# Optimization experiments

Measured on AMD Instinct MI355X. Metric: run time of the kernel, lower is better.

The kernel has to match this reference:

```python
import jax, jax.numpy as jnp
import numpy as np

EPS = 1e-5
NUM_GROUPS = 32
NUM_HEADS = 8

def group_norm(x, w, b):
    # x: (B, C, H, W), 32 groups, affine per-channel
    B, C, H, W = x.shape
    xg = x.reshape(B, NUM_GROUPS, C // NUM_GROUPS, H, W)
    mu = xg.mean(axis=(2, 3, 4), keepdims=True)
    var = xg.var(axis=(2, 3, 4), keepdims=True)
    xn = ((xg - mu) * jax.lax.rsqrt(var + EPS)).reshape(B, C, H, W)
    return xn * w[None, :, None, None] + b[None, :, None, None]

def conv1x1(x, w, b):
    # 1x1 conv == per-pixel linear; w: (out, in), x: (B, C, H, W)
    return jnp.einsum('oc,bchw->bohw', w, x) + b[None, :, None, None]

def setup_inputs() -> dict:
    key = jax.random.key(0)
    ks = jax.random.split(key, 4)
    B, C, H, W = 2, 512, 64, 64
    s = 1.0 / np.sqrt(C)
    return {
        'x': jax.random.normal(ks[0], (B, C, H, W), jnp.float32),
        'gn_w': jnp.ones((C,), jnp.float32),
        'gn_b': jnp.zeros((C,), jnp.float32),
        'wq': jax.random.normal(ks[1], (C, C), jnp.float32) * s,
        'bq': jnp.zeros((C,), jnp.float32),
        'wkv': jax.random.normal(ks[2], (2 * C, C), jnp.float32) * s,
        'bkv': jnp.zeros((2 * C,), jnp.float32),
        'wo': jax.random.normal(ks[3], (C, C), jnp.float32) * s,
        'bo': jnp.zeros((C,), jnp.float32),
    }

def reference(x, gn_w, gn_b, wq, bq, wkv, bkv, wo, bo):
    B, C, H, W = x.shape
    hd = C // NUM_HEADS  # head_dim
    residual = x
    x_norm = group_norm(x, gn_w, gn_b)
    q = conv1x1(x_norm, wq, bq).reshape(B, NUM_HEADS, hd, H * W)
    kv = conv1x1(x_norm, wkv, bkv)
    k, v = jnp.split(kv, 2, axis=1)
    k = k.reshape(B, NUM_HEADS, hd, H * W)
    v = v.reshape(B, NUM_HEADS, hd, H * W)
    scale = hd ** (-0.5)
    attn = jnp.einsum('bhdi,bhdj->bhij', q, k) * scale
    attn = jax.nn.softmax(attn, axis=-1)
    out = jnp.einsum('bhij,bhdj->bhdi', attn, v).reshape(B, C, H, W)
    out = conv1x1(out, wo, bo)
    return out + residual
```

## Files before the change

### kernel.cpp

```cpp
#include <hip/hip_runtime.h>
#include <cmath>

typedef __bf16 bf16x8 __attribute__((ext_vector_type(8)));
typedef __bf16 bf16x4 __attribute__((ext_vector_type(4)));
typedef float  f32x4  __attribute__((ext_vector_type(4)));
typedef unsigned uint2_ev __attribute__((ext_vector_type(2)));

static __device__ __forceinline__ f32x4 mfma16(bf16x8 a, bf16x8 b, f32x4 c) {
    return __builtin_amdgcn_mfma_f32_16x16x32_bf16(a, b, c, 0, 0, 0);
}

static __device__ __forceinline__ float fast_exp2(float x) {
#if __has_builtin(__builtin_amdgcn_exp2f)
    return __builtin_amdgcn_exp2f(x);
#else
    return exp2f(x);
#endif
}

static __device__ __forceinline__ void quad_swap(unsigned &a, unsigned &b) {
#if __has_builtin(__builtin_amdgcn_permlane32_swap) && __has_builtin(__builtin_amdgcn_permlane16_swap)
    uint2_ev r32 = __builtin_amdgcn_permlane32_swap(a, b, false, false);
    uint2_ev r16 = __builtin_amdgcn_permlane16_swap(r32[0], r32[1], false, false);
    a = r16[0]; b = r16[1];
#else
    asm volatile("v_permlane32_swap_b32 %0, %1\n\t"
                 "v_permlane16_swap_b32 %0, %1"
                 : "+v"(a), "+v"(b));
#endif
}

static __device__ __forceinline__ void gload_lds16(const void* g, void* l) {
    __builtin_amdgcn_global_load_lds((const __attribute__((address_space(1))) void*)g,
                                     (__attribute__((address_space(3))) void*)l, 16, 0, 0);
}

#define OFF_STATS 0
#define OFF_BEFF  1024
#define OFF_W     16384
#define OFF_XNT   (4u*1024*1024)
#define OFF_QKT   (OFF_XNT + 8u*1024*1024)
#define OFF_V     (OFF_QKT + 16u*1024*1024)
#define OFF_OP    (OFF_V + 8u*1024*1024)
#define CHUNK_O   4194304u
#define CHUNK_L   65536u

__global__ __launch_bounds__(256) void gn_fuse(const float* __restrict__ x,
                                               float* __restrict__ stats,
                                               __bf16* __restrict__ xT) {
    int p0 = blockIdx.x * 64, c0 = blockIdx.y * 64, b = blockIdx.z;
    int tid = threadIdx.x, lane = tid & 63, wave = tid >> 6;
    __shared__ float t[64][68];
    __shared__ float red[4][8];
    float acc_s[4] = {0.f,0.f,0.f,0.f}, acc_ss[4] = {0.f,0.f,0.f,0.f};
    const int rr = tid >> 4;
    const int p4 = (tid & 15) * 4;
    #pragma unroll
    for (int i = 0; i < 4; ++i) {
        int cc = rr + 16*i;
        float4 v = *(const float4*)&x[((size_t)(b*512 + c0 + cc) << 12) + p0 + p4];
        *(float4*)&t[cc][p4] = v;
        acc_s[i]  += v.x + v.y + v.z + v.w;
        acc_ss[i] += v.x*v.x + v.y*v.y + v.z*v.z + v.w*v.w;
    }
    #pragma unroll
    for (int g = 0; g < 4; ++g) {
        #pragma unroll
        for (int off = 1; off < 64; off <<= 1) {
            acc_s[g]  += __shfl_xor(acc_s[g],  off);
            acc_ss[g] += __shfl_xor(acc_ss[g], off);
        }
    }
    if (lane == 0) {
        #pragma unroll
        for (int g = 0; g < 4; ++g) { red[wave][g*2] = acc_s[g]; red[wave][g*2+1] = acc_ss[g]; }
    }
    __syncthreads();
    if (tid < 8) {
        float v0 = red[0][tid] + red[1][tid] + red[2][tid] + red[3][tid];
        int g = (b << 5) + (c0 >> 4) + (tid >> 1);
        atomicAdd(&stats[g*2 + (tid & 1)], v0);
    }
    const int ch = tid & 7;
    #pragma unroll
    for (int w = 0; w < 2; ++w) {
        int pp = (tid >> 3) + 32*w;
        __bf16 ob[8];
        #pragma unroll
        for (int e = 0; e < 8; ++e) ob[e] = (__bf16)t[ch*8 + e][pp];
        *(bf16x8*)&xT[((size_t)(b*4096 + p0 + pp) << 9) + c0 + ch*8] = *(bf16x8*)ob;
    }
}

__global__ __launch_bounds__(256) void prep_w(const float* __restrict__ wq,
                                              const float* __restrict__ wkv,
                                              const float* __restrict__ wo,
                                              const float* __restrict__ bq,
                                              const float* __restrict__ bkv,
                                              const float* __restrict__ stats,
                                              const float* __restrict__ gw,
                                              const float* __restrict__ gb,
                                              __bf16* __restrict__ wS,
                                              __bf16* __restrict__ wo_bf,
                                              float* __restrict__ beff) {
    const int b = blockIdx.y, bx = blockIdx.x;
    const int tid = threadIdx.x, lane = tid & 63, wave = tid >> 6;
    if (bx >= 48) {
        if (b) return;
        int r0 = (bx - 48) * 32;
        #pragma unroll
        for (int ps = 0; ps < 8; ++ps) {
            int row = r0 + ps*4 + wave;
            __bf16 obuf[8];
            #pragma unroll
            for (int e = 0; e < 8; ++e) obuf[e] = (__bf16)wo[(size_t)row*512 + lane*8 + e];
            *(bf16x8*)&wo_bf[(size_t)row*512 + lane*8] = *(bf16x8*)obuf;
        }
        return;
    }
    __shared__ float sS[512], sT[512];
    for (int c = tid; c < 512; c += 256) {
        int g = (b << 5) + (c >> 4);
        float mu   = stats[g*2] * (1.f/65536.f);
        float var  = stats[g*2+1] * (1.f/65536.f) - mu*mu;
        float rstd = rsqrtf(var + 1e-5f);
        float s = rstd * gw[c];
        sS[c] = s;
        sT[c] = gb[c] - mu * s;
    }
    __syncthreads();
    int r0 = bx * 32;
    #pragma unroll
    for (int ps = 0; ps < 8; ++ps) {
        int row = r0 + ps*4 + wave;
        const float* Wrow = (row < 512) ? (wq + (size_t)row*512) : (wkv + (size_t)(row-512)*512);
        float bias0 = (row < 512) ? bq[row] : bkv[row - 512];
        float bp = 0.f;
        __bf16 obuf[8];
        #pragma unroll
        for (int e = 0; e < 8; ++e) {
            int c = lane*8 + e;
            float wv_ = Wrow[c];
            obuf[e] = (__bf16)(wv_ * sS[c]);
            bp += wv_ * sT[c];
        }
        *(bf16x8*)&wS[((size_t)b*1536 + row)*512 + lane*8] = *(bf16x8*)obuf;
        #pragma unroll
        for (int off = 1; off < 64; off <<= 1) bp += __shfl_xor(bp, off);
        if (lane == 0) beff[b*1536 + row] = bias0 + bp;
    }
}

__global__ __launch_bounds__(256) void gemm128_kernel(
    const __bf16* __restrict__ A, const __bf16* __restrict__ B,
    const float* __restrict__ bias, int nsplit,
    float scale0, void* __restrict__ out, void* __restrict__ outV,
    int N, int K, long long strideA, long long strideB, long long strideO,
    long long strideV, int biasStride) {
    const int bz = blockIdx.z;
    A += strideA * bz;
    B += strideB * bz;
    const float* bb = bias + (size_t)bz * biasStride;
    const int m0 = blockIdx.x * 128, n0 = blockIdx.y * 128;
    const int tid = threadIdx.x, lane = tid & 63, wave = tid >> 6;
    const int quad = lane >> 4, l16 = lane & 15;
    const int wm = (wave >> 1) * 64, wn = (wave & 1) * 64;

    __shared__ __attribute__((aligned(16))) __bf16 lds_a[2][128][64];
    __shared__ __attribute__((aligned(16))) __bf16 lds_b[2][128][64];

    f32x4 acc[4][4];
    #pragma unroll
    for (int mt = 0; mt < 4; ++mt)
        #pragma unroll
        for (int nt = 0; nt < 4; ++nt)
            #pragma unroll
            for (int r = 0; r < 4; ++r) acc[mt][nt][r] = 0.f;

    const int myrow = (wave << 3) + (lane >> 3);
    const int mych  = ((lane & 7) ^ (myrow & 7)) << 3;
    const __bf16* Ab = A + (size_t)(m0 + myrow) * K + mych;
    const __bf16* Bb = B + (size_t)(n0 + myrow) * K + mych;

    auto stage = [&](int buf, int kt) {
        char* la = (char*)(&lds_a[buf][0][0]) + (wave << 10);
        char* lb = (char*)(&lds_b[buf][0][0]) + (wave << 10);
        #pragma unroll
        for (int i = 0; i < 4; ++i) {
            gload_lds16(Ab + kt + (size_t)(32*i) * K, la + i*4096);
            gload_lds16(Bb + kt + (size_t)(32*i) * K, lb + i*4096);
        }
    };

    stage(0, 0);
    const int NK = K >> 6;
    for (int k8 = 0; k8 < NK; ++k8) {
        __syncthreads();
        const int cur = k8 & 1;
        if (k8 + 1 < NK) stage(cur ^ 1, (k8 + 1) << 6);
        #pragma unroll
        for (int kh = 0; kh < 2; ++kh) {
            bf16x8 af[4], bfr[4];
            #pragma unroll
            for (int mt = 0; mt < 4; ++mt)
                af[mt] = *(const bf16x8*)&lds_a[cur][wm + mt*16 + l16][(((kh<<2)|quad) ^ (l16 & 7)) * 8];
            #pragma unroll
            for (int nt = 0; nt < 4; ++nt)
                bfr[nt] = *(const bf16x8*)&lds_b[cur][wn + nt*16 + l16][(((kh<<2)|quad) ^ (l16 & 7)) * 8];
            #pragma unroll
            for (int mt = 0; mt < 4; ++mt)
                #pragma unroll
                for (int nt = 0; nt < 4; ++nt)
                    acc[mt][nt] = mfma16(af[mt], bfr[nt], acc[mt][nt]);
        }
    }

    if (n0 < 1024) {
        #pragma unroll
        for (int mt = 0; mt < 4; ++mt) {
            const int mrow = m0 + wm + mt*16 + quad*4;
            #pragma unroll
            for (int nt = 0; nt < 4; ++nt) {
                const int ncol = n0 + wn + nt*16 + l16;
                #pragma unroll
                for (int r = 0; r < 4; ++r) {
                    const int m = mrow + r;
                    float val = acc[mt][nt][r] + bb[ncol];
                    if (ncol < nsplit) val *= scale0;
                    ((__bf16*)out)[(size_t)strideO * bz + (size_t)m * N + ncol] = (__bf16)val;
                }
            }
        }
    } else {
        __syncthreads();
        __bf16* T = (__bf16*)lds_a;
        #pragma unroll
        for (int mt = 0; mt < 4; ++mt) {
            const int pl  = wm + mt*16 + quad*4;
            const int pc  = pl >> 3;
            const int hlf = (pl >> 2) & 1;
            #pragma unroll
            for (int nt = 0; nt < 4; ++nt) {
                const int cl = wn + nt*16 + l16;
                const int ncol = n0 + cl;
                __bf16 ob[4];
                #pragma unroll
                for (int r = 0; r < 4; ++r)
                    ob[r] = (__bf16)(acc[mt][nt][r] + bb[ncol]);
                *(bf16x4*)&T[cl*128 + ((pc ^ (cl & 15)) << 3) + hlf*4] = *(bf16x4*)ob;
            }
        }
        __syncthreads();
        const int pch = tid & 15;
        __bf16* vvb = (__bf16*)outV + (size_t)strideV * bz;
        #pragma unroll
        for (int pass = 0; pass < 8; ++pass) {
            const int cl = pass*16 + (tid >> 4);
            bf16x8 vv8 = *(const bf16x8*)&T[cl*128 + ((pch ^ (cl & 15)) << 3)];
            *(bf16x8*)&vvb[(size_t)(n0 - 1024 + cl) * 4096 + m0 + pch*8] = vv8;
        }
    }
}

template<int OUT_F32, int HAS_RES>
__global__ __launch_bounds__(256) void gemm64_kernel(
    const __bf16* __restrict__ A, const __bf16* __restrict__ B,
    const float* __restrict__ bias, const float* __restrict__ res,
    void* __restrict__ out,
    int N, int K, long long strideA, long long strideB, long long strideO, int biasStride) {
    const int bz = blockIdx.z;
    A += strideA * bz;
    B += strideB * bz;
    const float* bb = bias + (size_t)bz * biasStride;
    const int m0 = blockIdx.x * 64, n0 = blockIdx.y * 128;
    const int tid = threadIdx.x, lane = tid & 63, wave = tid >> 6;
    const int quad = lane >> 4, l16 = lane & 15;
    const int wn = wave * 32;

    __shared__ __attribute__((aligned(16))) __bf16 lds_a[2][64][64];
    __shared__ __attribute__((aligned(16))) __bf16 lds_b[2][128][64];

    f32x4 acc[4][2];
    #pragma unroll
    for (int mt = 0; mt < 4; ++mt)
        #pragma unroll
        for (int nt = 0; nt < 2; ++nt)
            #pragma unroll
            for (int r = 0; r < 4; ++r) acc[mt][nt][r] = 0.f;

    const int myrow = (wave << 3) + (lane >> 3);
    const int mych  = ((lane & 7) ^ (myrow & 7)) << 3;
    const __bf16* Ab = A + (size_t)(m0 + myrow) * K + mych;
    const __bf16* Bb = B + (size_t)(n0 + myrow) * K + mych;

    auto stage = [&](int buf, int kt) {
        char* la = (char*)(&lds_a[buf][0][0]) + (wave << 10);
        char* lb = (char*)(&lds_b[buf][0][0]) + (wave << 10);
        #pragma unroll
        for (int i = 0; i < 2; ++i)
            gload_lds16(Ab + kt + (size_t)(32*i) * K, la + i*4096);
        #pragma unroll
        for (int i = 0; i < 4; ++i)
            gload_lds16(Bb + kt + (size_t)(32*i) * K, lb + i*4096);
    };

    stage(0, 0);
    const int NK = K >> 6;
    for (int k8 = 0; k8 < NK; ++k8) {
        __syncthreads();
        const int cur = k8 & 1;
        if (k8 + 1 < NK) stage(cur ^ 1, (k8 + 1) << 6);
        #pragma unroll
        for (int kh = 0; kh < 2; ++kh) {
            bf16x8 af[4], bfr[2];
            #pragma unroll
            for (int mt = 0; mt < 4; ++mt)
                af[mt] = *(const bf16x8*)&lds_a[cur][mt*16 + l16][(((kh<<2)|quad) ^ (l16 & 7)) * 8];
            #pragma unroll
            for (int nt = 0; nt < 2; ++nt)
                bfr[nt] = *(const bf16x8*)&lds_b[cur][wn + nt*16 + l16][(((kh<<2)|quad) ^ (l16 & 7)) * 8];
            #pragma unroll
            for (int mt = 0; mt < 4; ++mt)
                #pragma unroll
                for (int nt = 0; nt < 2; ++nt)
                    acc[mt][nt] = mfma16(af[mt], bfr[nt], acc[mt][nt]);
        }
    }

    #pragma unroll
    for (int mt = 0; mt < 4; ++mt) {
        const int mrow = m0 + mt*16 + quad*4;
        #pragma unroll
        for (int nt = 0; nt < 2; ++nt) {
            const int ncol = n0 + wn + nt*16 + l16;
            #pragma unroll
            for (int r = 0; r < 4; ++r) {
                const int m = mrow + r;
                float val = acc[mt][nt][r] + bb[m];
                const size_t idx = (size_t)strideO * bz + (size_t)m * N + ncol;
                if constexpr (HAS_RES) val += res[idx];
                if constexpr (OUT_F32) ((float*)out)[idx] = val;
                else ((__bf16*)out)[idx] = (__bf16)val;
            }
        }
    }
}

template<int NCH>
__global__ __launch_bounds__(256, 3) void attn_kernel(const __bf16* __restrict__ qkT,
                                                      const __bf16* __restrict__ v,
                                                      __bf16* __restrict__ attnT,
                                                      __bf16* __restrict__ Opart,
                                                      float* __restrict__ Lpart) {
    const int b = blockIdx.y >> 3, h = blockIdx.y & 7;
    const int chunk = (NCH > 1) ? blockIdx.z : 0;
    int NITER, kt0;
    if constexpr (NCH == 3) {
        NITER = (chunk == 0) ? 22 : 21;
        kt0   = (chunk == 0) ? 0 : (chunk == 1 ? 1408 : 2752);
    } else {
        NITER = 64 / NCH;
        kt0   = chunk * (4096 / NCH);
    }
    const int tid = threadIdx.x;
    const int wave = tid >> 6, lane = tid & 63;
    const int quad = lane >> 4, l16 = lane & 15;
    const int qbase = blockIdx.x * 256 + wave * 64;

    const __bf16* qkTb = qkT + ((size_t)b << 22);
    const __bf16* vb   = v   + ((size_t)b << 21);

    __shared__ __attribute__((aligned(16))) __bf16 lds_k[2][64][64];
    __shared__ __attribute__((aligned(16))) __bf16 lds_v[2][64][64];

    bf16x8 aq[4][2];
    #pragma unroll
    for (int mt = 0; mt < 4; ++mt) {
        const __bf16* qrow = qkTb + (size_t)(qbase + mt*16 + l16) * 1024 + h*64 + quad*8;
        aq[mt][0] = *(const bf16x8*)qrow;
        aq[mt][1] = *(const bf16x8*)(qrow + 32);
    }
    f32x4 o[4][5];
    #pragma unroll
    for (int mt = 0; mt < 4; ++mt)
        #pragma unroll
        for (int dt = 0; dt < 5; ++dt)
            #pragma unroll
            for (int r = 0; r < 4; ++r) o[mt][dt][r] = 0.f;
    const f32x4 kZero = {0.f, 0.f, 0.f, 0.f};

    bf16x8 onesb;
    #pragma unroll
    for (int e = 0; e < 8; ++e) onesb[e] = (__bf16)1.0f;

    const int myrow = (wave << 3) + (lane >> 3);
    const int mych  = ((lane & 7) ^ (myrow & 7)) << 3;
    const __bf16* kgb = qkTb + (size_t)myrow * 1024 + 512 + h*64 + mych;
    const __bf16* vgb = vb + ((size_t)(h*64 + myrow) << 12) + mych;

    auto stage = [&](int buf, int kt) {
        char* kb = (char*)(&lds_k[buf][0][0]) + (wave << 10);
        char* vp = (char*)(&lds_v[buf][0][0]) + (wave << 10);
        const __bf16* kg = kgb + (size_t)kt * 1024;
        const __bf16* vg = vgb + kt;
        gload_lds16(kg,                       kb);
        gload_lds16(kg + 32*1024,             kb + 4096);
        gload_lds16(vg,                       vp);
        gload_lds16(vg + ((size_t)32 << 12),  vp + 4096);
    };

    stage(0, kt0);

    for (int it = 0; it < NITER; ++it) {
        __syncthreads();
        const int cur = it & 1;
        if (it + 1 < NITER) stage(cur ^ 1, kt0 + (it + 1) * 64);

        #pragma unroll
        for (int kh = 0; kh < 2; ++kh) {
            __builtin_amdgcn_s_setprio(1);
            unsigned pd[4][4];
            #pragma unroll
            for (int j = 0; j < 2; ++j) {
                const int nt = kh*2 + j;
                const int kr = nt*16 + l16;
                bf16x8 bk0 = *(const bf16x8*)&lds_k[cur][kr][( quad      ^ (l16 & 7)) * 8];
                bf16x8 bk1 = *(const bf16x8*)&lds_k[cur][kr][((4 + quad) ^ (l16 & 7)) * 8];
                #pragma unroll
                for (int mt = 0; mt < 4; ++mt) {
                    f32x4 s = mfma16(bk1, aq[mt][1], mfma16(bk0, aq[mt][0], kZero));
                    f32x4 p;
                    #pragma unroll
                    for (int r = 0; r < 4; ++r) p[r] = fast_exp2(s[r]);
                    bf16x4 pb = __builtin_convertvector(p, bf16x4);
                    union { bf16x4 v; unsigned d[2]; } u; u.v = pb;
                    pd[mt][j*2]     = u.d[0];
                    pd[mt][j*2 + 1] = u.d[1];
                }
            }
            bf16x8 pa[4];
            #pragma unroll
            for (int mt = 0; mt < 4; ++mt) {
                unsigned x0 = pd[mt][0], x1 = pd[mt][1];
                unsigned y0 = pd[mt][2], y1 = pd[mt][3];
                quad_swap(x0, y0);
                quad_swap(x1, y1);
                union { unsigned d[4]; bf16x8 v; } u;
                u.d[0] = x0; u.d[1] = x1; u.d[2] = y0; u.d[3] = y1;
                pa[mt] = u.v;
            }
            #pragma unroll
            for (int dt = 0; dt < 4; ++dt) {
                bf16x8 bv = *(const bf16x8*)&lds_v[cur][dt*16 + l16][((kh*4 + quad) ^ (l16 & 7)) * 8];
                #pragma unroll
                for (int mt = 0; mt < 4; ++mt)
                    o[mt][dt] = mfma16(pa[mt], bv, o[mt][dt]);
            }
            #pragma unroll
            for (int mt = 0; mt < 4; ++mt)
                o[mt][4] = mfma16(pa[mt], onesb, o[mt][4]);
            __builtin_amdgcn_s_setprio(0);
        }
    }

    if constexpr (NCH > 1) {
        __bf16* Ob = Opart + (size_t)chunk * CHUNK_O;
        #pragma unroll
        for (int mt = 0; mt < 4; ++mt)
            #pragma unroll
            for (int dt = 0; dt < 4; ++dt)
                #pragma unroll
                for (int r = 0; r < 4; ++r) {
                    size_t row = (size_t)b * 4096 + qbase + mt*16 + quad*4 + r;
                    Ob[(row << 9) + (h << 6) + dt*16 + l16] = (__bf16)o[mt][dt][r];
                }
        if (l16 == 0) {
            #pragma unroll
            for (int mt = 0; mt < 4; ++mt)
                #pragma unroll
                for (int r = 0; r < 4; ++r) {
                    int p = qbase + mt*16 + quad*4 + r;
                    Lpart[(size_t)chunk * CHUNK_L + (size_t)(((b*8 + h)) << 12) + p] = o[mt][4][r];
                }
        }
    } else {
        #pragma unroll
        for (int mt = 0; mt < 4; ++mt) {
            float inv[4];
            #pragma unroll
            for (int r = 0; r < 4; ++r)
                inv[r] = 1.f / __shfl(o[mt][4][r], lane & 48);
            #pragma unroll
            for (int dt = 0; dt < 4; ++dt)
                #pragma unroll
                for (int r = 0; r < 4; ++r) {
                    size_t row = (size_t)b * 4096 + qbase + mt*16 + quad*4 + r;
                    attnT[(row << 9) + (h << 6) + dt*16 + l16] = (__bf16)(o[mt][dt][r] * inv[r]);
                }
        }
    }
}

template<int NCH>
__global__ __launch_bounds__(256) void attn_combine(const __bf16* __restrict__ Opart,
                                                    const float* __restrict__ Lpart,
                                                    __bf16* __restrict__ attnT) {
    int i = blockIdx.x * 256 + threadIdx.x;
    int c8 = i & 63;
    int p  = (i >> 6) & 4095;
    int b  = i >> 18;
    int h  = c8 >> 3;
    size_t lidx = (size_t)((b*8 + h) << 12) + p;
    float l = 0.f;
    #pragma unroll
    for (int ch = 0; ch < NCH; ++ch) l += Lpart[(size_t)ch * CHUNK_L + lidx];
    float inv = 1.f / l;
    size_t oi = ((size_t)(b*4096 + p) << 9) + c8*8;
    float acc[8] = {0.f,0.f,0.f,0.f,0.f,0.f,0.f,0.f};
    #pragma unroll
    for (int ch = 0; ch < NCH; ++ch) {
        bf16x8 ov = *(const bf16x8*)&Opart[(size_t)ch * CHUNK_O + oi];
        #pragma unroll
        for (int r = 0; r < 8; ++r) acc[r] += (float)ov[r];
    }
    bf16x8 rv;
    #pragma unroll
    for (int r = 0; r < 8; ++r) rv[r] = (__bf16)(acc[r] * inv);
    *(bf16x8*)&attnT[oi] = rv;
}

extern "C" void kernel_launch(void* const* d_in, const int* in_sizes, int n_in,
                              void* d_out, int out_size, void* d_ws, size_t ws_size,
                              hipStream_t stream) {
    const float* x   = (const float*)d_in[0];
    const float* gnw = (const float*)d_in[1];
    const float* gnb = (const float*)d_in[2];
    const float* wq  = (const float*)d_in[3];
    const float* bq  = (const float*)d_in[4];
    const float* wkv = (const float*)d_in[5];
    const float* bkv = (const float*)d_in[6];
    const float* wo  = (const float*)d_in[7];
    const float* bo  = (const float*)d_in[8];
    float* out = (float*)d_out;

    char* ws = (char*)d_ws;
    float*  stats  = (float*)(ws + OFF_STATS);
    float*  beff   = (float*)(ws + OFF_BEFF);
    __bf16* wS     = (__bf16*)(ws + OFF_W);
    __bf16* wo_bf  = wS + 2u*1536*512;
    __bf16* xT     = (__bf16*)(ws + OFF_XNT);
    __bf16* qkT    = (__bf16*)(ws + OFF_QKT);
    __bf16* vv     = (__bf16*)(ws + OFF_V);
    __bf16* Opart  = (__bf16*)(ws + OFF_OP);
    __bf16* attnT  = xT;

    const size_t need3 = (size_t)OFF_OP + 3u * (CHUNK_O * 2 + CHUNK_L * 4);
    const size_t need2 = (size_t)OFF_OP + 2u * (CHUNK_O * 2 + CHUNK_L * 4);
    const int nch = (ws_size >= need3) ? 3 : (ws_size >= need2 ? 2 : 1);
    float* Lpart = (float*)(ws + OFF_OP + (size_t)nch * CHUNK_O * 2);

    hipMemsetAsync(stats, 0, 512, stream);
    gn_fuse<<<dim3(64, 8, 2), 256, 0, stream>>>(x, stats, xT);
    prep_w<<<dim3(64, 2), 256, 0, stream>>>(wq, wkv, wo, bq, bkv, stats, gnw, gnb,
                                            wS, wo_bf, beff);

    const long long S  = 2097152LL;
    const long long S2 = 4194304LL;
    const long long SW = 1536LL*512;
    gemm128_kernel<<<dim3(32, 12, 2), 256, 0, stream>>>(
        xT, wS, beff, 512, 0.125f * 1.44269504f, qkT, vv, 1024, 512, S, SW, S2, S, 1536);

    if (nch == 3) {
        attn_kernel<3><<<dim3(16, 16, 3), 256, 0, stream>>>(qkT, vv, nullptr, Opart, Lpart);
        attn_combine<3><<<2048, 256, 0, stream>>>(Opart, Lpart, attnT);
    } else if (nch == 2) {
        attn_kernel<2><<<dim3(16, 16, 2), 256, 0, stream>>>(qkT, vv, nullptr, Opart, Lpart);
        attn_combine<2><<<2048, 256, 0, stream>>>(Opart, Lpart, attnT);
    } else {
        attn_kernel<1><<<dim3(16, 16, 1), 256, 0, stream>>>(qkT, vv, attnT, nullptr, nullptr);
    }

    gemm64_kernel<1,1><<<dim3(8, 32, 2), 256, 0, stream>>>(
        wo_bf, attnT, bo, x, out, 4096, 512, 0, S, S, 0);
}
```

Before: 209.0 us.

## Replace GN stat atomics with per-block partials and halve GEMM K-tile

Group-norm statistics are now written as per-block partial sums into a larger stats region and reduced in prep_w, which removes the memset launch and the float atomics. Separately, the QKV GEMM stages a K-slice of 32 instead of 64 per double-buffer step, halving shared memory per block (32KB instead of 64KB) to allow more resident blocks, at the cost of more barriers and loop iterations. Workspace offsets are moved to make room for the partials.

```diff
diff --git a/kernel.cpp b/kernel.cpp
--- a/kernel.cpp
+++ b/kernel.cpp
@@ -36,8 +36,8 @@
 }
 
 #define OFF_STATS 0
-#define OFF_BEFF  1024
-#define OFF_W     16384
+#define OFF_BEFF  32768
+#define OFF_W     49152
 #define OFF_XNT   (4u*1024*1024)
 #define OFF_QKT   (OFF_XNT + 8u*1024*1024)
 #define OFF_V     (OFF_QKT + 16u*1024*1024)
@@ -79,7 +79,7 @@
     if (tid < 8) {
         float v0 = red[0][tid] + red[1][tid] + red[2][tid] + red[3][tid];
         int g = (b << 5) + (c0 >> 4) + (tid >> 1);
-        atomicAdd(&stats[g*2 + (tid & 1)], v0);
+        stats[((size_t)g * 64 + blockIdx.x) * 2 + (tid & 1)] = v0;
     }
     const int ch = tid & 7;
     #pragma unroll
@@ -118,11 +118,21 @@
         }
         return;
     }
+    __shared__ float gsum[32][2];
     __shared__ float sS[512], sT[512];
+    if (tid < 64) {
+        int gl = tid >> 1, j = tid & 1;
+        const float* sp = stats + (((size_t)(b << 5) + gl) * 64) * 2 + j;
+        float s = 0.f;
+        #pragma unroll
+        for (int pb = 0; pb < 64; ++pb) s += sp[pb*2];
+        gsum[gl][j] = s;
+    }
+    __syncthreads();
     for (int c = tid; c < 512; c += 256) {
-        int g = (b << 5) + (c >> 4);
-        float mu   = stats[g*2] * (1.f/65536.f);
-        float var  = stats[g*2+1] * (1.f/65536.f) - mu*mu;
+        int gl = c >> 4;
+        float mu   = gsum[gl][0] * (1.f/65536.f);
+        float var  = gsum[gl][1] * (1.f/65536.f) - mu*mu;
         float rstd = rsqrtf(var + 1e-5f);
         float s = rstd * gw[c];
         sS[c] = s;
@@ -166,8 +176,9 @@
     const int quad = lane >> 4, l16 = lane & 15;
     const int wm = (wave >> 1) * 64, wn = (wave & 1) * 64;
 
-    __shared__ __attribute__((aligned(16))) __bf16 lds_a[2][128][64];
-    __shared__ __attribute__((aligned(16))) __bf16 lds_b[2][128][64];
+    __shared__ __attribute__((aligned(16))) __bf16 smem[16384];
+    __bf16 (*lds_a)[128][32] = (__bf16(*)[128][32])smem;
+    __bf16 (*lds_b)[128][32] = (__bf16(*)[128][32])(smem + 8192);
 
     f32x4 acc[4][4];
     #pragma unroll
@@ -177,42 +188,38 @@
             #pragma unroll
             for (int r = 0; r < 4; ++r) acc[mt][nt][r] = 0.f;
 
-    const int myrow = (wave << 3) + (lane >> 3);
-    const int mych  = ((lane & 7) ^ (myrow & 7)) << 3;
-    const __bf16* Ab = A + (size_t)(m0 + myrow) * K + mych;
-    const __bf16* Bb = B + (size_t)(n0 + myrow) * K + mych;
-
+    const int srow = (wave << 5) + (lane >> 2);
+    const int sch0 = ((lane & 3) ^ (srow & 3)) << 3;
     auto stage = [&](int buf, int kt) {
-        char* la = (char*)(&lds_a[buf][0][0]) + (wave << 10);
-        char* lb = (char*)(&lds_b[buf][0][0]) + (wave << 10);
-        #pragma unroll
-        for (int i = 0; i < 4; ++i) {
-            gload_lds16(Ab + kt + (size_t)(32*i) * K, la + i*4096);
-            gload_lds16(Bb + kt + (size_t)(32*i) * K, lb + i*4096);
+        char* la = (char*)(&lds_a[buf][0][0]) + (wave << 11);
+        char* lb = (char*)(&lds_b[buf][0][0]) + (wave << 11);
+        #pragma unroll
+        for (int i = 0; i < 2; ++i) {
+            const int r  = srow + (i << 4);
+            const int ch = ((lane & 3) ^ (r & 3)) << 3;
+            gload_lds16(A + (size_t)(m0 + r) * K + kt + ch, la + (i << 10));
+            gload_lds16(B + (size_t)(n0 + r) * K + kt + ch, lb + (i << 10));
         }
     };
 
     stage(0, 0);
-    const int NK = K >> 6;
-    for (int k8 = 0; k8 < NK; ++k8) {
+    const int NK = K >> 5;
+    for (int ks = 0; ks < NK; ++ks) {
         __syncthreads();
-        const int cur = k8 & 1;
-        if (k8 + 1 < NK) stage(cur ^ 1, (k8 + 1) << 6);
-        #pragma unroll
-        for (int kh = 0; kh < 2; ++kh) {
-            bf16x8 af[4], bfr[4];
-            #pragma unroll
-            for (int mt = 0; mt < 4; ++mt)
-                af[mt] = *(const bf16x8*)&lds_a[cur][wm + mt*16 + l16][(((kh<<2)|quad) ^ (l16 & 7)) * 8];
+        const int cur = ks & 1;
+        if (ks + 1 < NK) stage(cur ^ 1, (ks + 1) << 5);
+        bf16x8 af[4], bfr[4];
+        #pragma unroll
+        for (int mt = 0; mt < 4; ++mt)
+            af[mt] = *(const bf16x8*)&lds_a[cur][wm + mt*16 + l16][(quad ^ (l16 & 3)) * 8];
+        #pragma unroll
+        for (int nt = 0; nt < 4; ++nt)
+            bfr[nt] = *(const bf16x8*)&lds_b[cur][wn + nt*16 + l16][(quad ^ (l16 & 3)) * 8];
+        #pragma unroll
+        for (int mt = 0; mt < 4; ++mt)
             #pragma unroll
             for (int nt = 0; nt < 4; ++nt)
-                bfr[nt] = *(const bf16x8*)&lds_b[cur][wn + nt*16 + l16][(((kh<<2)|quad) ^ (l16 & 7)) * 8];
-            #pragma unroll
-            for (int mt = 0; mt < 4; ++mt)
-                #pragma unroll
-                for (int nt = 0; nt < 4; ++nt)
-                    acc[mt][nt] = mfma16(af[mt], bfr[nt], acc[mt][nt]);
-        }
+                acc[mt][nt] = mfma16(af[mt], bfr[nt], acc[mt][nt]);
     }
 
     if (n0 < 1024) {
@@ -233,7 +240,7 @@
         }
     } else {
         __syncthreads();
-        __bf16* T = (__bf16*)lds_a;
+        __bf16* T = smem;
         #pragma unroll
         for (int mt = 0; mt < 4; ++mt) {
             const int pl  = wm + mt*16 + quad*4;
@@ -559,7 +566,6 @@
     const int nch = (ws_size >= need3) ? 3 : (ws_size >= need2 ? 2 : 1);
     float* Lpart = (float*)(ws + OFF_OP + (size_t)nch * CHUNK_O * 2);
 
-    hipMemsetAsync(stats, 0, 512, stream);
     gn_fuse<<<dim3(64, 8, 2), 256, 0, stream>>>(x, stats, xT);
     prep_w<<<dim3(64, 2), 256, 0, stream>>>(wq, wkv, wo, bq, bkv, stats, gnw, gnb,
                                             wS, wo_bf, beff);
```

Measured after the change: 213.2 us. About the same (+2.0%).
